# Performance work log

Measured on AMD Instinct MI355X. Metric: run time of the kernel, lower is better.

Reference implementation:

```python
import jax, jax.numpy as jnp
import numpy as np
from jax import lax

B, L, N, C_IN = 32, 12, 4096, 4
HIDDEN, GRID = 64, 8
N_STEPS, DT = 10, 0.1  # euler odeint, t in [0,1], step_size=0.1


def setup_inputs() -> dict:
    key = jax.random.key(0)
    ks = jax.random.split(key, 16)
    history_data = jax.random.normal(ks[0], (B, L, N, C_IN), dtype=jnp.float32)
    x0 = jax.random.normal(ks[1], (B, L, N, 1), dtype=jnp.float32)  # ODE init noise
    # orthonormal graph spectral basis (eigenvectors of graph Laplacian)
    U, _ = jnp.linalg.qr(jax.random.normal(ks[2], (N, N), dtype=jnp.float32))
    # KASA backbone stand-in: temporal mixing over the 12 input steps of channel 0
    Wk = jax.random.normal(ks[3], (L, L), dtype=jnp.float32) * 0.1
    bk = jnp.zeros((1, L, 1, 1), dtype=jnp.float32)
    # 1x1 conv adapter over the L=12 'channel' axis (zero-init in torch; random here so compute is live)
    Wad = jax.random.normal(ks[4], (L, L), dtype=jnp.float32) * 0.05
    bad = jnp.zeros((1, L, 1, 1), dtype=jnp.float32)
    kasa_gate = jnp.asarray(0.3, dtype=jnp.float32)
    fm_gate = jnp.asarray(0.5, dtype=jnp.float32)  # nonzero so the ODE sampling branch runs
    # Fourier-KAN vector field: 3 input feats (x_t, cond_spec, t) -> hidden -> 1
    A1 = jax.random.normal(ks[5], (HIDDEN, 3, GRID), dtype=jnp.float32) * (1.0 / np.sqrt(3 * GRID))
    B1 = jax.random.normal(ks[6], (HIDDEN, 3, GRID), dtype=jnp.float32) * (1.0 / np.sqrt(3 * GRID))
    b1 = jnp.zeros((HIDDEN,), dtype=jnp.float32)
    W2 = jax.random.normal(ks[7], (HIDDEN, 1), dtype=jnp.float32) * (1.0 / np.sqrt(HIDDEN))
    b2 = jnp.zeros((1,), dtype=jnp.float32)
    return {"history_data": history_data, "x0": x0, "U": U, "Wk": Wk, "bk": bk,
            "Wad": Wad, "bad": bad, "kasa_gate": kasa_gate, "fm_gate": fm_gate,
            "A1": A1, "B1": B1, "b1": b1, "W2": W2, "b2": b2}


def _vector_field(x, t, cond, A1, B1, b1, W2, b2):
    # x, cond: [B,L,N,1]; t: scalar
    tf = jnp.broadcast_to(jnp.asarray(t, x.dtype), x.shape)
    feat = jnp.concatenate([x, cond, tf], axis=-1)  # [B,L,N,3]
    freqs = jnp.arange(1, GRID + 1, dtype=x.dtype)
    ang = feat[..., None] * freqs  # [B,L,N,3,G]
    h = (jnp.einsum('blnig,hig->blnh', jnp.cos(ang), A1)
         + jnp.einsum('blnig,hig->blnh', jnp.sin(ang), B1) + b1)
    h = jax.nn.silu(h)
    return h @ W2 + b2  # [B,L,N,1]


def _forward(history_data, x0, U, Wk, bk, Wad, bad, kasa_gate, fm_gate, A1, B1, b1, W2, b2):
    n = U.shape[0]
    scale = jnp.sqrt(jnp.asarray(n, jnp.float32))
    # prior baseline: last step, channel 3, repeated over 12 horizon steps
    prior = jnp.broadcast_to(history_data[:, -1:, :, 3:4], (history_data.shape[0], L, n, 1))
    # KASA backbone stand-in + 1x1 conv adapter over L channels
    kasa_raw = jnp.einsum('btnc,lt->blnc', history_data[..., 0:1], Wk) + bk
    adapter_out = jnp.einsum('blnc,ol->bonc', kasa_raw, Wad) + bad
    base_pred = prior + jnp.tanh(adapter_out) * kasa_gate
    # GFT: U^T x along node axis, scaled
    cond_spec = jnp.einsum('nm,blnc->blmc', U, base_pred) / scale
    # fixed-step Euler flow-matching sampler, t = 0.0 .. 0.9
    def step(x, k):
        t = DT * k.astype(jnp.float32)
        v = _vector_field(x, t, cond_spec, A1, B1, b1, W2, b2)
        return x + DT * v, None
    x_final, _ = lax.scan(step, x0, jnp.arange(N_STEPS))
    # IGFT: U x_hat, undo scaling
    gen_residual = jnp.einsum('mn,blnc->blmc', U, x_final * scale)
    return base_pred + fm_gate * gen_residual


def reference(history_data, x0, U, Wk, bk, Wad, bad, kasa_gate, fm_gate, A1, B1, b1, W2, b2):
    return _forward(history_data, x0, U, Wk, bk, Wad, bad, kasa_gate, fm_gate, A1, B1, b1, W2, b2)
```

## Files before the change

### kernel.cpp

```cpp
#include <hip/hip_runtime.h>
#include <hip/hip_bf16.h>
#include <math.h>

#define BB 32
#define LL 12
#define NN 4096
#define CIN 4
#define HID 64
#define GRID_F 8
#define NSTEP 10
#define DTS 0.1f
#define BLN (BB*LL)
#define ELEMS (BB*LL*NN)
#define K4 4096

#define L2E 1.4426950408889634f
#define LN2 0.6931471805599453f

typedef __attribute__((ext_vector_type(8))) short short8;
typedef __attribute__((ext_vector_type(16))) float f32x16;
typedef __attribute__((ext_vector_type(2))) float f32x2;

union FragU { unsigned u[4]; uint4 v; short8 s; };
union BF2U { __hip_bfloat162 h; unsigned u; };

__device__ __forceinline__ unsigned pack2bf(float a, float b) {
    unsigned ua = __float_as_uint(a);
    unsigned ub = __float_as_uint(b);
    ua += 0x7FFFu + ((ua >> 16) & 1u);
    ub += 0x7FFFu + ((ub >> 16) & 1u);
    return (ua & 0xFFFF0000u) | (ub >> 16);
}

__device__ __forceinline__ unsigned short bf16of(float a) {
    unsigned ua = __float_as_uint(a);
    ua += 0x7FFFu + ((ua >> 16) & 1u);
    return (unsigned short)(ua >> 16);
}

__device__ __forceinline__ f32x16 fzero16() {
    f32x16 z;
#pragma unroll
    for (int i = 0; i < 16; ++i) z[i] = 0.f;
    return z;
}

__global__ __launch_bounds__(256) void base_pred_kernel(
    const float* __restrict__ hd,
    const float* __restrict__ Wk,
    const float* __restrict__ bk,
    const float* __restrict__ Wad,
    const float* __restrict__ bad,
    const float* __restrict__ kgp,
    float* __restrict__ base,
    unsigned short* __restrict__ base16)
{
    int idx = blockIdx.x * 256 + threadIdx.x;
    int b = idx >> 12;
    int n = idx & 4095;
    const float* hb = hd + (size_t)b * (LL * NN * CIN) + (size_t)n * CIN;

    float h0[12];
    float prior = 0.f;
#pragma unroll
    for (int t = 0; t < 12; ++t) {
        float4 v = *reinterpret_cast<const float4*>(hb + (size_t)t * (NN * CIN));
        h0[t] = v.x;
        if (t == 11) prior = v.w;
    }
    float kgate = kgp[0];

    float kr[12];
#pragma unroll
    for (int l = 0; l < 12; ++l) {
        float p = bk[l];
#pragma unroll
        for (int t = 0; t < 12; ++t) p = fmaf(h0[t], Wk[l * 12 + t], p);
        kr[l] = p;
    }
#pragma unroll
    for (int o = 0; o < 12; ++o) {
        float p = bad[o];
#pragma unroll
        for (int l = 0; l < 12; ++l) p = fmaf(kr[l], Wad[o * 12 + l], p);
        float val = prior + tanhf(p) * kgate;
        size_t off = ((size_t)(b * 12 + o)) * NN + n;
        base[off] = val;
        if (base16) base16[off] = bf16of(val);
    }
}

__global__ void tfeat_kernel(unsigned short* __restrict__ tf16)
{
    int idx = blockIdx.x * blockDim.x + threadIdx.x;
    if (idx >= NSTEP * 16) return;
    int k = idx >> 4;
    int r = idx & 15;
    int hi = r >> 3;
    int j = r & 7;
    float ang = DTS * (float)k * (float)(j + 1);
    float v = hi ? sinf(ang) : cosf(ang);
    tf16[idx] = bf16of(v);
}

__global__ __launch_bounds__(256) void u_convert_kernel(
    const float* __restrict__ U,
    unsigned short* __restrict__ U16,
    unsigned short* __restrict__ UT16)
{
    __shared__ unsigned short tile[64][66];
    const int t = threadIdx.x;
    const int bx = blockIdx.x;
    const int by = blockIdx.y;
    {
        int r  = t >> 2;
        int c0 = (t & 3) * 16;
        size_t gr = (size_t)(by * 64 + r);
        size_t gc = (size_t)(bx * 64) + c0;
        const float4* src = reinterpret_cast<const float4*>(U + gr * K4 + gc);
        unsigned ou[8];
#pragma unroll
        for (int i = 0; i < 4; ++i) {
            float4 v = src[i];
            ou[2 * i]     = pack2bf(v.y, v.x);
            ou[2 * i + 1] = pack2bf(v.w, v.z);
        }
        uint4* dst = reinterpret_cast<uint4*>(&U16[gr * K4 + gc]);
        dst[0] = make_uint4(ou[0], ou[1], ou[2], ou[3]);
        dst[1] = make_uint4(ou[4], ou[5], ou[6], ou[7]);
#pragma unroll
        for (int i = 0; i < 8; ++i) {
            tile[r][c0 + 2 * i]     = (unsigned short)(ou[i] & 0xFFFFu);
            tile[r][c0 + 2 * i + 1] = (unsigned short)(ou[i] >> 16);
        }
    }
    __syncthreads();
    {
        int c  = t >> 2;
        int r0 = (t & 3) * 16;
        unsigned ou[8];
#pragma unroll
        for (int i = 0; i < 8; ++i) {
            unsigned lo = tile[r0 + 2 * i][c];
            unsigned hi = tile[r0 + 2 * i + 1][c];
            ou[i] = lo | (hi << 16);
        }
        size_t gm = (size_t)(bx * 64 + c);
        size_t gn = (size_t)(by * 64) + r0;
        uint4* dst = reinterpret_cast<uint4*>(&UT16[gm * K4 + gn]);
        dst[0] = make_uint4(ou[0], ou[1], ou[2], ou[3]);
        dst[1] = make_uint4(ou[4], ou[5], ou[6], ou[7]);
    }
}

template <bool TRANS_STORE>
__global__ __launch_bounds__(256) void gemm_mfma64(
    const unsigned short* __restrict__ A,
    const unsigned short* __restrict__ Bt,
    const float* __restrict__ C0,
    float* __restrict__ C,
    const float* __restrict__ alpha_ptr,
    float alpha_const)
{
    __shared__ uint4 lds4[2][1024];
    unsigned char* ldsc = reinterpret_cast<unsigned char*>(&lds4[0][0]);

    const int tid  = threadIdx.x;
    const int lane = tid & 63;
    const int l31  = lane & 31;
    const int hi   = lane >> 5;
    const int w    = tid >> 6;
    const int wr   = w >> 1;
    const int wc   = w & 1;
    const int m0   = blockIdx.y * 64;
    const int n0   = blockIdx.x * 64;

    const int srow = tid >> 1;
    const int skb  = (tid & 1) * 64;
    const bool isB = srow >= 64;
    const int  rloc = srow & 63;
    const unsigned char* gsrc = (isB ? (const unsigned char*)Bt + ((size_t)(n0 + rloc) * K4) * 2
                                     : (const unsigned char*)A  + ((size_t)(m0 + rloc) * K4) * 2) + skb;
    const int swbase = (isB ? 8192 : 0) + rloc * 128;
    const int sswz   = (rloc & 7) << 4;

    uint4 rg[4];
    auto LOADG = [&](int kt) {
        const size_t kby = (size_t)kt * 128;
#pragma unroll
        for (int i = 0; i < 4; ++i)
            rg[i] = *reinterpret_cast<const uint4*>(gsrc + kby + i * 16);
    };
    auto WRITE_LDS = [&](int buf) {
        unsigned char* p = ldsc + buf * 16384;
#pragma unroll
        for (int i = 0; i < 4; ++i)
            *reinterpret_cast<uint4*>(p + (swbase + ((skb + i * 16) ^ sswz))) = rg[i];
    };

    f32x16 acc = fzero16();

    const int raw = wr * 32 + l31;
    const int rbw = wc * 32 + l31;
    const int khb = hi * 16;
    const int aswz = (raw & 7) << 4;
    const int bswz = (rbw & 7) << 4;

    LOADG(0);
    WRITE_LDS(0);

    for (int kt = 0; kt < K4 / 64; ++kt) {
        __syncthreads();
        if (kt + 1 < K4 / 64) LOADG(kt + 1);
        const unsigned char* p = ldsc + (kt & 1) * 16384;
#pragma unroll
        for (int ks = 0; ks < 4; ++ks) {
            const int kc = ks * 32 + khb;
            short8 a = *reinterpret_cast<const short8*>(p + (raw * 128 + (kc ^ aswz)));
            short8 b = *reinterpret_cast<const short8*>(p + 8192 + (rbw * 128 + (kc ^ bswz)));
            acc = __builtin_amdgcn_mfma_f32_32x32x16_bf16(a, b, acc, 0, 0, 0);
        }
        if (kt + 1 < K4 / 64) WRITE_LDS((kt + 1) & 1);
    }

    float alpha = alpha_const;
    if (alpha_ptr) alpha *= alpha_ptr[0];

    if (!TRANS_STORE) {
        int colg = n0 + wc * 32 + l31;
        int rowb = m0 + wr * 32 + 4 * hi;
#pragma unroll
        for (int r = 0; r < 16; ++r) {
            int row = rowb + (r & 3) + 8 * (r >> 2);
            C[(size_t)row * K4 + colg] = acc[r] * alpha;
        }
    } else {
        int rowo = n0 + wc * 32 + l31;
        int mb   = m0 + wr * 32 + 4 * hi;
#pragma unroll
        for (int q = 0; q < 4; ++q) {
            size_t off = (size_t)rowo * K4 + mb + 8 * q;
            float4 c0v = *reinterpret_cast<const float4*>(&C0[off]);
            float4 v;
            v.x = fmaf(acc[4 * q + 0], alpha, c0v.x);
            v.y = fmaf(acc[4 * q + 1], alpha, c0v.y);
            v.z = fmaf(acc[4 * q + 2], alpha, c0v.z);
            v.w = fmaf(acc[4 * q + 3], alpha, c0v.w);
            *reinterpret_cast<float4*>(&C[off]) = v;
        }
    }
}

#define GMT 64
#define GNT 64
#define GKT 32
#define GPAD 4

template <bool UT>
__global__ __launch_bounds__(256) void gemm_u(
    const float* __restrict__ X,
    const float* __restrict__ Uq,
    const float* __restrict__ C0,
    float* __restrict__ C,
    const float* __restrict__ alpha_ptr,
    float alpha_const)
{
    __shared__ float Xs[GKT][GMT + GPAD];
    __shared__ float Us[GKT][GNT + GPAD];

    const int t = threadIdx.x;
    const int m0 = blockIdx.y * GMT;
    const int n0 = blockIdx.x * GNT;
    const int tx = t & 15;
    const int ty = t >> 4;
    const int srow = t >> 2;
    const int scol = (t & 3) * 8;

    float acc[4][4] = {};

    for (int k0 = 0; k0 < NN; k0 += GKT) {
        {
            const float4* xp = reinterpret_cast<const float4*>(
                &X[(size_t)(m0 + srow) * NN + k0 + scol]);
            float4 a = xp[0], b4 = xp[1];
            Xs[scol + 0][srow] = a.x;  Xs[scol + 1][srow] = a.y;
            Xs[scol + 2][srow] = a.z;  Xs[scol + 3][srow] = a.w;
            Xs[scol + 4][srow] = b4.x; Xs[scol + 5][srow] = b4.y;
            Xs[scol + 6][srow] = b4.z; Xs[scol + 7][srow] = b4.w;
        }
        if (UT) {
            int kk = t >> 3;
            int j0 = (t & 7) * 8;
            const float4* up = reinterpret_cast<const float4*>(
                &Uq[(size_t)(k0 + kk) * NN + n0 + j0]);
            float4 a = up[0], b4 = up[1];
            Us[kk][j0 + 0] = a.x;  Us[kk][j0 + 1] = a.y;
            Us[kk][j0 + 2] = a.z;  Us[kk][j0 + 3] = a.w;
            Us[kk][j0 + 4] = b4.x; Us[kk][j0 + 5] = b4.y;
            Us[kk][j0 + 6] = b4.z; Us[kk][j0 + 7] = b4.w;
        } else {
            const float4* up = reinterpret_cast<const float4*>(
                &Uq[(size_t)(n0 + srow) * NN + k0 + scol]);
            float4 a = up[0], b4 = up[1];
            Us[scol + 0][srow] = a.x;  Us[scol + 1][srow] = a.y;
            Us[scol + 2][srow] = a.z;  Us[scol + 3][srow] = a.w;
            Us[scol + 4][srow] = b4.x; Us[scol + 5][srow] = b4.y;
            Us[scol + 6][srow] = b4.z; Us[scol + 7][srow] = b4.w;
        }
        __syncthreads();
#pragma unroll
        for (int kk = 0; kk < GKT; ++kk) {
            float a[4], bb[4];
#pragma unroll
            for (int i = 0; i < 4; ++i) a[i] = Xs[kk][ty * 4 + i];
#pragma unroll
            for (int j = 0; j < 4; ++j) bb[j] = Us[kk][tx * 4 + j];
#pragma unroll
            for (int i = 0; i < 4; ++i)
#pragma unroll
                for (int j = 0; j < 4; ++j)
                    acc[i][j] = fmaf(a[i], bb[j], acc[i][j]);
        }
        __syncthreads();
    }

    float alpha = alpha_const;
    if (alpha_ptr) alpha *= alpha_ptr[0];

#pragma unroll
    for (int i = 0; i < 4; ++i) {
        int row = m0 + ty * 4 + i;
        size_t off = (size_t)row * NN + n0 + tx * 4;
        float4 v;
        v.x = acc[i][0] * alpha;
        v.y = acc[i][1] * alpha;
        v.z = acc[i][2] * alpha;
        v.w = acc[i][3] * alpha;
        if (C0) {
            float4 c0 = *reinterpret_cast<const float4*>(&C0[off]);
            v.x += c0.x; v.y += c0.y; v.z += c0.z; v.w += c0.w;
        }
        *reinterpret_cast<float4*>(&C[off]) = v;
    }
}

__global__ __launch_bounds__(256) void ode_kernel(
    const float* __restrict__ x0,
    float* __restrict__ xc,
    const unsigned short* __restrict__ tf16,
    const float* __restrict__ A1,
    const float* __restrict__ B1,
    const float* __restrict__ b1,
    const float* __restrict__ W2,
    const float* __restrict__ b2,
    unsigned short* __restrict__ xf16)
{
    const int tid  = threadIdx.x;
    const int lane = tid & 63;
    const int e31  = lane & 31;
    const int hi   = lane >> 5;
    const int wv   = tid >> 6;
    const size_t eg = (size_t)blockIdx.x * 128 + (size_t)wv * 32 + e31;

    FragU af[2][3];
#pragma unroll
    for (int mt = 0; mt < 2; ++mt) {
        int h = mt * 32 + e31;
#pragma unroll
        for (int c = 0; c < 3; ++c) {
            const float* wp = (hi ? B1 : A1) + (size_t)(h * 3 + c) * 8;
            float4 f0 = *reinterpret_cast<const float4*>(wp);
            float4 f1 = *reinterpret_cast<const float4*>(wp + 4);
            af[mt][c].u[0] = pack2bf(f0.y * L2E, f0.x * L2E);
            af[mt][c].u[1] = pack2bf(f0.w * L2E, f0.z * L2E);
            af[mt][c].u[2] = pack2bf(f1.y * L2E, f1.x * L2E);
            af[mt][c].u[3] = pack2bf(f1.w * L2E, f1.z * L2E);
        }
    }

    f32x16 ci0, ci1;
    f32x2 w2p0[8], w2p1[8];
#pragma unroll
    for (int r = 0; r < 16; ++r) {
        int row = (r & 3) + 8 * (r >> 2) + 4 * hi;
        ci0[r] = b1[row] * L2E;
        ci1[r] = b1[32 + row] * L2E;
        float w0 = W2[row] * LN2;
        float w1 = W2[32 + row] * LN2;
        if (r & 1) { w2p0[r >> 1].y = w0; w2p1[r >> 1].y = w1; }
        else       { w2p0[r >> 1].x = w0; w2p1[r >> 1].x = w1; }
    }

    float x   = x0[eg];
    float cnd = xc[eg];
    const float db2 = DTS * b2[0];

    FragU bc;
    {
        float s, c;
        __sincosf(cnd, &s, &c);
        float cg[8], sg[8];
        cg[0] = c; sg[0] = s;
#pragma unroll
        for (int g = 1; g < 8; ++g) {
            cg[g] = cg[g - 1] * c - sg[g - 1] * s;
            sg[g] = sg[g - 1] * c + cg[g - 1] * s;
        }
#pragma unroll
        for (int t = 0; t < 4; ++t) {
            float a0 = hi ? sg[2 * t]     : cg[2 * t];
            float a1 = hi ? sg[2 * t + 1] : cg[2 * t + 1];
            bc.u[t] = pack2bf(a1, a0);
        }
    }

#pragma unroll 1
    for (int k = 0; k < NSTEP; ++k) {
        FragU bt;
        bt.v = *reinterpret_cast<const uint4*>(tf16 + k * 16 + hi * 8);

        float s, c;
        __sincosf(x, &s, &c);
        float cg[8], sg[8];
        cg[0] = c; sg[0] = s;
#pragma unroll
        for (int g = 1; g < 8; ++g) {
            cg[g] = cg[g - 1] * c - sg[g - 1] * s;
            sg[g] = sg[g - 1] * c + cg[g - 1] * s;
        }
        FragU bx;
#pragma unroll
        for (int t = 0; t < 4; ++t) {
            BF2U cv;
            float a0f = hi ? sg[2 * t]     : cg[2 * t];
            float a1f = hi ? sg[2 * t + 1] : cg[2 * t + 1];
            cv.h = __float22bfloat162_rn(make_float2(a0f, a1f));
            bx.u[t] = cv.u;
        }

        f32x2 dA = {0.f, 0.f}, dB = {0.f, 0.f};

        {
            f32x16 aa = __builtin_amdgcn_mfma_f32_32x32x16_bf16(af[0][0].s, bx.s, ci0, 0, 0, 0);
            aa = __builtin_amdgcn_mfma_f32_32x32x16_bf16(af[0][1].s, bc.s, aa, 0, 0, 0);
            aa = __builtin_amdgcn_mfma_f32_32x32x16_bf16(af[0][2].s, bt.s, aa, 0, 0, 0);

            f32x2 e[8];
#pragma unroll
            for (int p = 0; p < 8; ++p) {
                e[p].x = __builtin_amdgcn_exp2f(-aa[2 * p]);
                e[p].y = __builtin_amdgcn_exp2f(-aa[2 * p + 1]);
            }
#pragma unroll
            for (int p = 0; p < 8; ++p) e[p] = e[p] + 1.0f;
#pragma unroll
            for (int p = 0; p < 8; ++p) {
                e[p].x = __builtin_amdgcn_rcpf(e[p].x);
                e[p].y = __builtin_amdgcn_rcpf(e[p].y);
            }
#pragma unroll
            for (int p = 0; p < 8; ++p) {
                f32x2 q; q.x = aa[2 * p]; q.y = aa[2 * p + 1];
                f32x2 m = q * w2p0[p];
                if (p & 1) dB = m * e[p] + dB;
                else       dA = m * e[p] + dA;
            }
        }

        {
            f32x16 aa = __builtin_amdgcn_mfma_f32_32x32x16_bf16(af[1][0].s, bx.s, ci1, 0, 0, 0);
            aa = __builtin_amdgcn_mfma_f32_32x32x16_bf16(af[1][1].s, bc.s, aa, 0, 0, 0);
            aa = __builtin_amdgcn_mfma_f32_32x32x16_bf16(af[1][2].s, bt.s, aa, 0, 0, 0);

            f32x2 e[8];
#pragma unroll
            for (int p = 0; p < 8; ++p) {
                e[p].x = __builtin_amdgcn_exp2f(-aa[2 * p]);
                e[p].y = __builtin_amdgcn_exp2f(-aa[2 * p + 1]);
            }
#pragma unroll
            for (int p = 0; p < 8; ++p) e[p] = e[p] + 1.0f;
#pragma unroll
            for (int p = 0; p < 8; ++p) {
                e[p].x = __builtin_amdgcn_rcpf(e[p].x);
                e[p].y = __builtin_amdgcn_rcpf(e[p].y);
            }
#pragma unroll
            for (int p = 0; p < 8; ++p) {
                f32x2 q; q.x = aa[2 * p]; q.y = aa[2 * p + 1];
                f32x2 m = q * w2p1[p];
                if (p & 1) dB = m * e[p] + dB;
                else       dA = m * e[p] + dA;
            }
        }

        f32x2 dd = dA + dB;
        float dot = dd.x + dd.y;
        float other = __shfl_xor(dot, 32, 64);
        dot += other;
        x = fmaf(DTS, dot, x) + db2;
    }

    if (xf16) {
        if (!hi) xf16[eg] = bf16of(x);
    } else {
        if (!hi) xc[eg] = x;
    }
}

extern "C" void kernel_launch(void* const* d_in, const int* in_sizes, int n_in,
                              void* d_out, int out_size, void* d_ws, size_t ws_size,
                              hipStream_t stream) {
    const float* hd  = (const float*)d_in[0];
    const float* x0  = (const float*)d_in[1];
    const float* U   = (const float*)d_in[2];
    const float* Wk  = (const float*)d_in[3];
    const float* bk  = (const float*)d_in[4];
    const float* Wad = (const float*)d_in[5];
    const float* bad = (const float*)d_in[6];
    const float* kg  = (const float*)d_in[7];
    const float* fg  = (const float*)d_in[8];
    const float* A1  = (const float*)d_in[9];
    const float* B1  = (const float*)d_in[10];
    const float* b1  = (const float*)d_in[11];
    const float* W2  = (const float*)d_in[12];
    const float* b2  = (const float*)d_in[13];
    float* out = (float*)d_out;

    unsigned char* ws = (unsigned char*)d_ws;
    const size_t offBase = 0;
    const size_t offXC   = 6291456;
    const size_t offTF   = 12582912;
    const size_t offB16  = 12583936;
    const size_t offXF   = 15729664;
    const size_t offU16  = 18875392;
    const size_t offUT   = 52429824;
    const size_t needFast = 85984256;

    float* base = (float*)(ws + offBase);
    float* xc   = (float*)(ws + offXC);
    unsigned short* tf16 = (unsigned short*)(ws + offTF);

    const bool fast = (ws_size >= needFast);

    if (fast) {
        unsigned short* base16 = (unsigned short*)(ws + offB16);
        unsigned short* xf16   = (unsigned short*)(ws + offXF);
        unsigned short* U16    = (unsigned short*)(ws + offU16);
        unsigned short* UT16   = (unsigned short*)(ws + offUT);

        u_convert_kernel<<<dim3(64, 64), 256, 0, stream>>>(U, U16, UT16);
        base_pred_kernel<<<(BB * NN) / 256, 256, 0, stream>>>(
            hd, Wk, bk, Wad, bad, kg, base, base16);
        tfeat_kernel<<<1, 256, 0, stream>>>(tf16);
        gemm_mfma64<false><<<dim3(NN / 64, BLN / 64), 256, 0, stream>>>(
            base16, UT16, nullptr, xc, nullptr, 1.0f / 64.0f);
        ode_kernel<<<ELEMS / 128, 256, 0, stream>>>(
            x0, xc, tf16, A1, B1, b1, W2, b2, xf16);
        gemm_mfma64<true><<<dim3(BLN / 64, NN / 64), 256, 0, stream>>>(
            U16, xf16, base, out, fg, 64.0f);
    } else {
        base_pred_kernel<<<(BB * NN) / 256, 256, 0, stream>>>(
            hd, Wk, bk, Wad, bad, kg, base, nullptr);
        tfeat_kernel<<<1, 256, 0, stream>>>(tf16);
        gemm_u<true><<<dim3(NN / GNT, BLN / GMT), 256, 0, stream>>>(
            base, U, nullptr, xc, nullptr, 1.0f / 64.0f);
        ode_kernel<<<ELEMS / 128, 256, 0, stream>>>(
            x0, xc, tf16, A1, B1, b1, W2, b2, nullptr);
        gemm_u<false><<<dim3(NN / GNT, BLN / GMT), 256, 0, stream>>>(
            xc, U, base, out, fg, 64.0f);
    }
}
```

Baseline: 509.5 us.

## Merge prep kernels into one launch and deepen GEMM global prefetch

The U conversion/transpose, base prediction and time-feature kernels are combined into a single launch that dispatches by block index, which removes two launches and lets the small jobs run alongside the large U conversion. The MFMA GEMM now keeps two register stages of global loads, so the tile loaded two iterations ahead is in flight while the current tile is computed, and the LDS write moves to the top of the loop. The extra register buffer raises register pressure, and the new ordering depends on the existing barrier to avoid overwriting LDS that is still being read.

```diff
diff --git a/kernel.cpp b/kernel.cpp
--- a/kernel.cpp
+++ b/kernel.cpp
@@ -43,6 +43,113 @@
 #pragma unroll
     for (int i = 0; i < 16; ++i) z[i] = 0.f;
     return z;
+}
+
+__global__ __launch_bounds__(256) void prep_kernel(
+    const float* __restrict__ U,
+    unsigned short* __restrict__ U16,
+    unsigned short* __restrict__ UT16,
+    const float* __restrict__ hd,
+    const float* __restrict__ Wk,
+    const float* __restrict__ bk,
+    const float* __restrict__ Wad,
+    const float* __restrict__ bad,
+    const float* __restrict__ kgp,
+    float* __restrict__ base,
+    unsigned short* __restrict__ base16,
+    unsigned short* __restrict__ tf16)
+{
+    __shared__ unsigned short tile[64][66];
+    const int bid = blockIdx.x;
+    const int t = threadIdx.x;
+
+    if (bid < 4096) {
+        const int bx = bid & 63;
+        const int by = bid >> 6;
+        {
+            int r  = t >> 2;
+            int c0 = (t & 3) * 16;
+            size_t gr = (size_t)(by * 64 + r);
+            size_t gc = (size_t)(bx * 64) + c0;
+            const float4* src = reinterpret_cast<const float4*>(U + gr * K4 + gc);
+            unsigned ou[8];
+#pragma unroll
+            for (int i = 0; i < 4; ++i) {
+                float4 v = src[i];
+                ou[2 * i]     = pack2bf(v.y, v.x);
+                ou[2 * i + 1] = pack2bf(v.w, v.z);
+            }
+            uint4* dst = reinterpret_cast<uint4*>(&U16[gr * K4 + gc]);
+            dst[0] = make_uint4(ou[0], ou[1], ou[2], ou[3]);
+            dst[1] = make_uint4(ou[4], ou[5], ou[6], ou[7]);
+#pragma unroll
+            for (int i = 0; i < 8; ++i) {
+                tile[r][c0 + 2 * i]     = (unsigned short)(ou[i] & 0xFFFFu);
+                tile[r][c0 + 2 * i + 1] = (unsigned short)(ou[i] >> 16);
+            }
+        }
+        __syncthreads();
+        {
+            int c  = t >> 2;
+            int r0 = (t & 3) * 16;
+            unsigned ou[8];
+#pragma unroll
+            for (int i = 0; i < 8; ++i) {
+                unsigned lo = tile[r0 + 2 * i][c];
+                unsigned hi = tile[r0 + 2 * i + 1][c];
+                ou[i] = lo | (hi << 16);
+            }
+            size_t gm = (size_t)(bx * 64 + c);
+            size_t gn = (size_t)(by * 64) + r0;
+            uint4* dst = reinterpret_cast<uint4*>(&UT16[gm * K4 + gn]);
+            dst[0] = make_uint4(ou[0], ou[1], ou[2], ou[3]);
+            dst[1] = make_uint4(ou[4], ou[5], ou[6], ou[7]);
+        }
+    } else if (bid < 4096 + 512) {
+        int idx = (bid - 4096) * 256 + t;
+        int b = idx >> 12;
+        int n = idx & 4095;
+        const float* hb = hd + (size_t)b * (LL * NN * CIN) + (size_t)n * CIN;
+
+        float h0[12];
+        float prior = 0.f;
+#pragma unroll
+        for (int tt = 0; tt < 12; ++tt) {
+            float4 v = *reinterpret_cast<const float4*>(hb + (size_t)tt * (NN * CIN));
+            h0[tt] = v.x;
+            if (tt == 11) prior = v.w;
+        }
+        float kgate = kgp[0];
+
+        float kr[12];
+#pragma unroll
+        for (int l = 0; l < 12; ++l) {
+            float p = bk[l];
+#pragma unroll
+            for (int tt = 0; tt < 12; ++tt) p = fmaf(h0[tt], Wk[l * 12 + tt], p);
+            kr[l] = p;
+        }
+#pragma unroll
+        for (int o = 0; o < 12; ++o) {
+            float p = bad[o];
+#pragma unroll
+            for (int l = 0; l < 12; ++l) p = fmaf(kr[l], Wad[o * 12 + l], p);
+            float val = prior + tanhf(p) * kgate;
+            size_t off = ((size_t)(b * 12 + o)) * NN + n;
+            base[off] = val;
+            base16[off] = bf16of(val);
+        }
+    } else {
+        if (t < NSTEP * 16) {
+            int k = t >> 4;
+            int r = t & 15;
+            int hi = r >> 3;
+            int j = r & 7;
+            float ang = DTS * (float)k * (float)(j + 1);
+            float v = hi ? sinf(ang) : cosf(ang);
+            tf16[t] = bf16of(v);
+        }
+    }
 }
 
 __global__ __launch_bounds__(256) void base_pred_kernel(
@@ -103,56 +210,6 @@
     tf16[idx] = bf16of(v);
 }
 
-__global__ __launch_bounds__(256) void u_convert_kernel(
-    const float* __restrict__ U,
-    unsigned short* __restrict__ U16,
-    unsigned short* __restrict__ UT16)
-{
-    __shared__ unsigned short tile[64][66];
-    const int t = threadIdx.x;
-    const int bx = blockIdx.x;
-    const int by = blockIdx.y;
-    {
-        int r  = t >> 2;
-        int c0 = (t & 3) * 16;
-        size_t gr = (size_t)(by * 64 + r);
-        size_t gc = (size_t)(bx * 64) + c0;
-        const float4* src = reinterpret_cast<const float4*>(U + gr * K4 + gc);
-        unsigned ou[8];
-#pragma unroll
-        for (int i = 0; i < 4; ++i) {
-            float4 v = src[i];
-            ou[2 * i]     = pack2bf(v.y, v.x);
-            ou[2 * i + 1] = pack2bf(v.w, v.z);
-        }
-        uint4* dst = reinterpret_cast<uint4*>(&U16[gr * K4 + gc]);
-        dst[0] = make_uint4(ou[0], ou[1], ou[2], ou[3]);
-        dst[1] = make_uint4(ou[4], ou[5], ou[6], ou[7]);
-#pragma unroll
-        for (int i = 0; i < 8; ++i) {
-            tile[r][c0 + 2 * i]     = (unsigned short)(ou[i] & 0xFFFFu);
-            tile[r][c0 + 2 * i + 1] = (unsigned short)(ou[i] >> 16);
-        }
-    }
-    __syncthreads();
-    {
-        int c  = t >> 2;
-        int r0 = (t & 3) * 16;
-        unsigned ou[8];
-#pragma unroll
-        for (int i = 0; i < 8; ++i) {
-            unsigned lo = tile[r0 + 2 * i][c];
-            unsigned hi = tile[r0 + 2 * i + 1][c];
-            ou[i] = lo | (hi << 16);
-        }
-        size_t gm = (size_t)(bx * 64 + c);
-        size_t gn = (size_t)(by * 64) + r0;
-        uint4* dst = reinterpret_cast<uint4*>(&UT16[gm * K4 + gn]);
-        dst[0] = make_uint4(ou[0], ou[1], ou[2], ou[3]);
-        dst[1] = make_uint4(ou[4], ou[5], ou[6], ou[7]);
-    }
-}
-
 template <bool TRANS_STORE>
 __global__ __launch_bounds__(256) void gemm_mfma64(
     const unsigned short* __restrict__ A,
@@ -184,18 +241,18 @@
     const int swbase = (isB ? 8192 : 0) + rloc * 128;
     const int sswz   = (rloc & 7) << 4;
 
-    uint4 rg[4];
-    auto LOADG = [&](int kt) {
+    uint4 rg[2][4];
+    auto LOADG = [&](uint4* r, int kt) {
         const size_t kby = (size_t)kt * 128;
 #pragma unroll
         for (int i = 0; i < 4; ++i)
-            rg[i] = *reinterpret_cast<const uint4*>(gsrc + kby + i * 16);
+            r[i] = *reinterpret_cast<const uint4*>(gsrc + kby + i * 16);
     };
-    auto WRITE_LDS = [&](int buf) {
+    auto WRITE_LDS = [&](int buf, const uint4* r) {
         unsigned char* p = ldsc + buf * 16384;
 #pragma unroll
         for (int i = 0; i < 4; ++i)
-            *reinterpret_cast<uint4*>(p + (swbase + ((skb + i * 16) ^ sswz))) = rg[i];
+            *reinterpret_cast<uint4*>(p + (swbase + ((skb + i * 16) ^ sswz))) = r[i];
     };
 
     f32x16 acc = fzero16();
@@ -205,13 +262,17 @@
     const int khb = hi * 16;
     const int aswz = (raw & 7) << 4;
     const int bswz = (rbw & 7) << 4;
-
-    LOADG(0);
-    WRITE_LDS(0);
-
-    for (int kt = 0; kt < K4 / 64; ++kt) {
+    const int NT = K4 / 64;
+
+    LOADG(rg[0], 0);
+    WRITE_LDS(0, rg[0]);
+    LOADG(rg[1], 1);
+
+    for (int kt = 0; kt < NT; ++kt) {
         __syncthreads();
-        if (kt + 1 < K4 / 64) LOADG(kt + 1);
+        if (kt + 1 < NT) WRITE_LDS((kt + 1) & 1, rg[(kt + 1) & 1]);
+        if (kt + 2 < NT) LOADG(rg[kt & 1], kt + 2);
+
         const unsigned char* p = ldsc + (kt & 1) * 16384;
 #pragma unroll
         for (int ks = 0; ks < 4; ++ks) {
@@ -220,7 +281,6 @@
             short8 b = *reinterpret_cast<const short8*>(p + 8192 + (rbw * 128 + (kc ^ bswz)));
             acc = __builtin_amdgcn_mfma_f32_32x32x16_bf16(a, b, acc, 0, 0, 0);
         }
-        if (kt + 1 < K4 / 64) WRITE_LDS((kt + 1) & 1);
     }
 
     float alpha = alpha_const;
@@ -549,10 +609,8 @@
         unsigned short* U16    = (unsigned short*)(ws + offU16);
         unsigned short* UT16   = (unsigned short*)(ws + offUT);
 
-        u_convert_kernel<<<dim3(64, 64), 256, 0, stream>>>(U, U16, UT16);
-        base_pred_kernel<<<(BB * NN) / 256, 256, 0, stream>>>(
-            hd, Wk, bk, Wad, bad, kg, base, base16);
-        tfeat_kernel<<<1, 256, 0, stream>>>(tf16);
+        prep_kernel<<<4096 + 512 + 1, 256, 0, stream>>>(
+            U, U16, UT16, hd, Wk, bk, Wad, bad, kg, base, base16, tf16);
         gemm_mfma64<false><<<dim3(NN / 64, BLN / 64), 256, 0, stream>>>(
             base16, UT16, nullptr, xc, nullptr, 1.0f / 64.0f);
         ode_kernel<<<ELEMS / 128, 256, 0, stream>>>(
```

New measurement: 595.9 us. 1.17x slower.
